# Optimization experiments

Measured on AMD Instinct MI355X. Metric: run time of the kernel, lower is better.

The kernel has to match this reference:

```python
import jax, jax.numpy as jnp
import numpy as np

NEG_INF = -9e15  # matches torch's -9000000000000000.0 mask fill
LEAKY_SLOPE = 0.01  # F.leaky_relu default


def setup_inputs() -> dict:
    key = jax.random.key(0)
    ks = jax.random.split(key, 6)
    B, N, F_in, F_out = 4, 4096, 256, 128
    h = jax.random.normal(ks[0], (B, N, F_in), dtype=jnp.float32)
    adj = jax.random.randint(ks[1], (B, N, N), 0, 2, dtype=jnp.int32)
    W_w = jax.random.normal(ks[2], (F_out, F_in), dtype=jnp.float32) * (1.0 / np.sqrt(F_in))
    W_b = jax.random.normal(ks[3], (F_out,), dtype=jnp.float32) * 0.01
    a_w = jax.random.normal(ks[4], (2 * F_out,), dtype=jnp.float32) * (1.0 / np.sqrt(2 * F_out))
    a_b = jax.random.normal(ks[5], (), dtype=jnp.float32) * 0.01
    return {"h": h, "adj": adj, "W_w": W_w, "W_b": W_b, "a_w": a_w, "a_b": a_b}


def reference(h, adj, W_w, W_b, a_w, a_b):
    # Wh: [B, N, F_out]
    Wh = jnp.einsum('bnf,of->bno', h, W_w) + W_b
    F_out = Wh.shape[-1]
    # a([Wh_i, Wh_j]) decomposes as a_src.Wh_i + a_dst.Wh_j + a_b (linearity),
    # avoiding the O(N^2 * 2F) repeat+cat intermediate while computing identical math.
    a_src, a_dst = a_w[:F_out], a_w[F_out:]
    src = jnp.einsum('bno,o->bn', Wh, a_src)  # [B, N]
    dst = jnp.einsum('bno,o->bn', Wh, a_dst)  # [B, N]
    e = src[:, :, None] + dst[:, None, :] + a_b  # [B, N, N]
    e = jnp.where(e >= 0, e, LEAKY_SLOPE * e)  # leaky_relu
    masked = jnp.where(adj > 0, e, NEG_INF)
    attention = jax.nn.softmax(masked, axis=-1)  # row softmax over neighbors j
    h_prime = jnp.einsum('bij,bjo->bio', attention, Wh)
    return h_prime
```

## Files before the change

kernel.cpp:

```cpp
#include <hip/hip_runtime.h>
#include <hip/hip_bf16.h>

typedef __attribute__((ext_vector_type(4))) float f32x4;
typedef __attribute__((ext_vector_type(8))) short s16x8;
typedef unsigned long long u64;

#define NB_ 4
#define N_ 4096
#define FI_ 256
#define FO_ 128
#define NROWS 16384
#define SPLIT 4
#define PHC 128
#define NST ((N_ / SPLIT) / PHC)

__device__ __forceinline__ unsigned pkbf(float a, float b) {
    __hip_bfloat162 t = __float22bfloat162_rn(make_float2(a, b));
    unsigned r; __builtin_memcpy(&r, &t, 4); return r;
}

typedef __attribute__((address_space(1))) const void CGV;
typedef __attribute__((address_space(3))) void LDSV;
__device__ __forceinline__ void gload16(const void* g, void* l) {
    __builtin_amdgcn_global_load_lds((CGV*)g, (LDSV*)l, 16, 0, 0);
}

__global__ __launch_bounds__(256) void k0_packw(
    const float* __restrict__ Ww, __hip_bfloat16* __restrict__ whi,
    __hip_bfloat16* __restrict__ wlo)
{
    int idx = blockIdx.x * 256 + threadIdx.x;
    float v = Ww[idx];
    __hip_bfloat16 hi = __float2bfloat16(v);
    whi[idx] = hi;
    wlo[idx] = __float2bfloat16(v - __bfloat162float(hi));
}

__global__ __launch_bounds__(256) void k1_wh(
    const float* __restrict__ h, const __hip_bfloat16* __restrict__ whi,
    const __hip_bfloat16* __restrict__ wlo, const float* __restrict__ Wb,
    const float* __restrict__ aw, const float* __restrict__ ab,
    short* __restrict__ WhTf, float* __restrict__ srcv,
    float* __restrict__ dstbv, unsigned* __restrict__ auxp)
{
    __shared__ float lds[16][132];
    const int tid = threadIdx.x;
    const int w = tid >> 6, l = tid & 63;
    const int lr = l & 15, g = l >> 4;
    const int r0 = blockIdx.x * 16;
    const float* hp = h + (size_t)(r0 + lr) * FI_ + g * 8;

    f32x4 acc[2] = {(f32x4)0.f, (f32x4)0.f};

    #pragma unroll
    for (int kt = 0; kt < 8; ++kt) {
        f32x4 x0 = *(const f32x4*)(hp + kt * 32);
        f32x4 x1 = *(const f32x4*)(hp + kt * 32 + 4);
        float xx[8];
        #pragma unroll
        for (int t = 0; t < 4; ++t) { xx[t] = x0[t]; xx[t + 4] = x1[t]; }
        union { s16x8 v; unsigned u[4]; } ahi, alo;
        #pragma unroll
        for (int t = 0; t < 4; ++t) {
            float a0 = xx[2 * t], a1 = xx[2 * t + 1];
            unsigned uh = pkbf(a0, a1);
            ahi.u[t] = uh;
            float h0f = __uint_as_float(uh << 16);
            float h1f = __uint_as_float(uh & 0xffff0000u);
            alo.u[t] = pkbf(a0 - h0f, a1 - h1f);
        }
        #pragma unroll
        for (int c = 0; c < 2; ++c) {
            const int o = w * 32 + c * 16 + lr;
            s16x8 bh = *(const s16x8*)(whi + (size_t)o * FI_ + kt * 32 + g * 8);
            s16x8 bl = *(const s16x8*)(wlo + (size_t)o * FI_ + kt * 32 + g * 8);
            acc[c] = __builtin_amdgcn_mfma_f32_16x16x32_bf16(ahi.v, bh, acc[c], 0, 0, 0);
            acc[c] = __builtin_amdgcn_mfma_f32_16x16x32_bf16(alo.v, bh, acc[c], 0, 0, 0);
            acc[c] = __builtin_amdgcn_mfma_f32_16x16x32_bf16(ahi.v, bl, acc[c], 0, 0, 0);
        }
    }

    #pragma unroll
    for (int c = 0; c < 2; ++c) {
        int col = w * 32 + c * 16 + lr;
        float wb = Wb[col];
        #pragma unroll
        for (int kk = 0; kk < 4; ++kk)
            lds[g * 4 + kk][col] = acc[c][kk] + wb;
    }
    __syncthreads();

    {
        const int o = tid >> 1, joct = tid & 1;
        const int jblk = (r0 & 4095) >> 5;
        const int bb = r0 >> 12;
        const int lb = ((r0 >> 3) & 3) + joct;
        union { s16x8 v; unsigned u[4]; } af;
        #pragma unroll
        for (int q = 0; q < 4; ++q)
            af.u[q] = pkbf(lds[joct * 8 + 2 * q][o], lds[joct * 8 + 2 * q + 1][o]);
        short* dst = WhTf + (((size_t)bb * 128 + jblk) * 8 + (o >> 4)) * 512
                          + ((o & 15) + 16 * lb) * 8;
        *(s16x8*)dst = af.v;
    }

    {
        const int row = tid >> 4, seg = tid & 15;
        float sp = 0.f, dp = 0.f;
        #pragma unroll
        for (int i = 0; i < 8; ++i) {
            float v = lds[row][seg * 8 + i];
            sp += v * aw[seg * 8 + i];
            dp += v * aw[FO_ + seg * 8 + i];
        }
        #pragma unroll
        for (int off = 8; off >= 1; off >>= 1) {
            sp += __shfl_xor(sp, off);
            dp += __shfl_xor(dp, off);
        }
        if (seg == 0) {
            int r = r0 + row;
            srcv[r] = sp;
            float db = dp + ab[0];
            dstbv[r] = db;
            auxp[r] = pkbf(__expf(db), __expf(0.01f * db));
        }
    }
}

__global__ __launch_bounds__(256) void k2b_max(
    const float* __restrict__ dstbv, float* __restrict__ maxv)
{
    const int b = blockIdx.x;
    const int t = threadIdx.x, w = t >> 6, l = t & 63;
    float m = -3.4e38f;
    for (int i = t; i < N_; i += 256) m = fmaxf(m, dstbv[b * N_ + i]);
    #pragma unroll
    for (int off = 32; off >= 1; off >>= 1) m = fmaxf(m, __shfl_xor(m, off));
    __shared__ float red[4];
    if (l == 0) red[w] = m;
    __syncthreads();
    if (t == 0) maxv[b] = fmaxf(fmaxf(red[0], red[1]), fmaxf(red[2], red[3]));
}

__global__ __launch_bounds__(256, 4) void k3_gat(
    const int* __restrict__ adj, const short* __restrict__ WhTf,
    const float* __restrict__ srcv, const unsigned* __restrict__ auxp,
    const float* __restrict__ maxv, float* __restrict__ pacc,
    float* __restrict__ prow)
{
    __shared__ int adjb[2][32][128];
    __shared__ float rsum[32];

    const int t = threadIdx.x;
    const int w = t >> 6, l = t & 63;
    const int lr = l & 15, g = l >> 4;
    const int rh = w & 1, oh = w >> 1;
    const int b = blockIdx.x >> 7;
    const int rblk = (blockIdx.x & 127) * 32;
    const int bN = b * N_;
    const int j0 = blockIdx.y * (N_ / SPLIT);

    float C1, C2;
    {
        int r = rblk + rh * 16 + lr;
        float s = srcv[bN + r];
        float eub = s + maxv[b];
        float m = fmaxf(eub, 0.01f * eub);
        C1 = __expf(s - m);
        C2 = __expf(0.01f * s - m);
    }

    const unsigned* axp = auxp + (size_t)bN + j0 + g * 8;
    const short* whsrc = WhTf + ((size_t)b * 128 + (j0 >> 5)) * 4096;

    f32x4 acc[4];
    #pragma unroll
    for (int ot = 0; ot < 4; ++ot) acc[ot] = (f32x4)0.f;
    float rs = 0.f;

    auto stage_adj = [&](int bi, int s) {
        const int jb = j0 + s * PHC;
        #pragma unroll
        for (int i = 0; i < 4; ++i) {
            int slot = i * 64 + (t & 63) + (t >> 6) * 256;
            int r = (i * 256 + t) >> 5;
            int c = (i * 256 + t) & 31;
            const int* src = adj + (size_t)(bN + rblk + r) * N_ + jb
                                 + ((c ^ (r & 7)) << 2);
            (void)slot;
            gload16(src, &adjb[bi][0][0] + (size_t)(i * 256 + w * 64) * 4);
        }
    };

    stage_adj(0, 0);
    __syncthreads();
    int cur = 0;

    for (int s = 0; s < NST; ++s) {
        if (s + 1 < NST) stage_adj(cur ^ 1, s + 1);

        #pragma unroll
        for (int js = 0; js < 4; ++js) {
            const int jc = s * PHC + js * 32;
            uint4 x0 = *(const uint4*)(axp + jc);
            uint4 x1 = *(const uint4*)(axp + jc + 4);
            const short* bp = whsrc + (size_t)(s * 4 + js) * 4096;
            s16x8 Bf[4];
            #pragma unroll
            for (int ot = 0; ot < 4; ++ot)
                Bf[ot] = *(const s16x8*)(bp + (oh * 4 + ot) * 512 + l * 8);

            const int R = rh * 16 + lr;
            const int c0 = js * 8 + 2 * g;
            const int4 a0 = *(const int4*)&adjb[cur][R][(c0 ^ (R & 7)) << 2];
            const int4 a1 = *(const int4*)&adjb[cur][R][((c0 + 1) ^ (R & 7)) << 2];

            const unsigned ax[8] = {x0.x, x0.y, x0.z, x0.w, x1.x, x1.y, x1.z, x1.w};
            const int av[8] = {a0.x, a0.y, a0.z, a0.w, a1.x, a1.y, a1.z, a1.w};
            float p[8];
            #pragma unroll
            for (int e = 0; e < 8; ++e) {
                float e1f = __uint_as_float(ax[e] << 16);
                float e2f = __uint_as_float(ax[e] & 0xffff0000u);
                float v = fmaxf(e1f * C1, e2f * C2);
                p[e] = (av[e] > 0) ? v : 0.f;
                rs += p[e];
            }
            union { s16x8 v; unsigned u[4]; } af;
            af.u[0] = pkbf(p[0], p[1]); af.u[1] = pkbf(p[2], p[3]);
            af.u[2] = pkbf(p[4], p[5]); af.u[3] = pkbf(p[6], p[7]);

            #pragma unroll
            for (int ot = 0; ot < 4; ++ot)
                acc[ot] = __builtin_amdgcn_mfma_f32_16x16x32_bf16(
                    af.v, Bf[ot], acc[ot], 0, 0, 0);
        }

        __syncthreads();
        cur ^= 1;
    }

    rs += __shfl_xor(rs, 16);
    rs += __shfl_xor(rs, 32);
    if (oh == 0 && l < 16) rsum[rh * 16 + l] = rs;
    __syncthreads();

    const size_t sb = (size_t)blockIdx.y * ((size_t)NROWS * FO_);
    #pragma unroll
    for (int kk = 0; kk < 4; ++kk) {
        int rloc = rh * 16 + g * 4 + kk;
        int grow = bN + rblk + rloc;
        float* pp = pacc + sb + (size_t)grow * FO_ + oh * 64 + lr;
        #pragma unroll
        for (int ot = 0; ot < 4; ++ot)
            pp[ot * 16] = acc[ot][kk];
        if (oh == 0 && lr == 0)
            prow[blockIdx.y * NROWS + grow] = rsum[rloc];
    }
}

__global__ __launch_bounds__(256) void k4_comb(
    const float* __restrict__ pacc, const float* __restrict__ prow,
    float* __restrict__ out)
{
    const int idx = blockIdx.x * 256 + threadIdx.x;
    const int grow = idx >> 7;
    float s = 0.f, rs = 0.f;
    #pragma unroll
    for (int si = 0; si < SPLIT; ++si) {
        s  += pacc[(size_t)si * ((size_t)NROWS * FO_) + idx];
        rs += prow[si * NROWS + grow];
    }
    out[idx] = s / rs;
}

extern "C" void kernel_launch(void* const* d_in, const int* in_sizes, int n_in,
                              void* d_out, int out_size, void* d_ws, size_t ws_size,
                              hipStream_t stream)
{
    const float* h  = (const float*)d_in[0];
    const int* adj  = (const int*)d_in[1];
    const float* Ww = (const float*)d_in[2];
    const float* Wb = (const float*)d_in[3];
    const float* aw = (const float*)d_in[4];
    const float* ab = (const float*)d_in[5];
    float* out = (float*)d_out;

    char* wsb = (char*)d_ws;
    float* pacc          = (float*)wsb;
    short* WhTf          = (short*)(wsb + 33554432u);
    char* aux            = wsb + 37748736u;
    float* srcv          = (float*)(aux);
    float* dstbv         = (float*)(aux + (64u << 10));
    unsigned* auxp       = (unsigned*)(aux + (128u << 10));
    __hip_bfloat16* whi  = (__hip_bfloat16*)(aux + (192u << 10));
    __hip_bfloat16* wlo  = (__hip_bfloat16*)(aux + (256u << 10));
    float* maxv          = (float*)(aux + (320u << 10));
    float* prow          = (float*)(aux + (384u << 10));

    k0_packw<<<128, 256, 0, stream>>>(Ww, whi, wlo);
    k1_wh<<<1024, 256, 0, stream>>>(h, whi, wlo, Wb, aw, ab, WhTf, srcv, dstbv, auxp);
    k2b_max<<<4, 256, 0, stream>>>(dstbv, maxv);
    dim3 g3(NB_ * 128, SPLIT);
    k3_gat<<<g3, 256, 0, stream>>>(adj, WhTf, srcv, auxp, maxv, pacc, prow);
    k4_comb<<<8192, 256, 0, stream>>>(pacc, prow, out);
}
```

Before: 142.9 us.

## Fuse dst max into Wh kernel via atomics and stage Wh/aux through LDS pipeline

Drops the separate max-reduction kernel: k1 now folds each block's dst max into a per-batch atomicMax on an order-preserving unsigned encoding, with a memset before launch. k3 moves to 32-column steps and stages adj (triple buffered), Wh tiles and aux values into LDS using async global-to-LDS loads, ordered with explicit vmcnt waits and barriers. This replaces direct global reads of B operands inside the loop. It also removes the LDS row-sum exchange by writing row sums directly. The aim is to hide global latency and save a launch, at the cost of one barrier per smaller step and hand-counted waitcnt correctness.

```diff
diff --git a/kernel.cpp b/kernel.cpp
--- a/kernel.cpp
+++ b/kernel.cpp
@@ -11,8 +11,7 @@
 #define FO_ 128
 #define NROWS 16384
 #define SPLIT 4
-#define PHC 128
-#define NST ((N_ / SPLIT) / PHC)
+#define NSTEPS ((N_ / SPLIT) / 32)
 
 __device__ __forceinline__ unsigned pkbf(float a, float b) {
     __hip_bfloat162 t = __float22bfloat162_rn(make_float2(a, b));
@@ -23,6 +22,15 @@
 typedef __attribute__((address_space(3))) void LDSV;
 __device__ __forceinline__ void gload16(const void* g, void* l) {
     __builtin_amdgcn_global_load_lds((CGV*)g, (LDSV*)l, 16, 0, 0);
+}
+
+__device__ __forceinline__ unsigned encf(float x) {
+    unsigned u = __float_as_uint(x);
+    return (u & 0x80000000u) ? ~u : (u | 0x80000000u);
+}
+__device__ __forceinline__ float decf(unsigned v) {
+    unsigned u = (v & 0x80000000u) ? (v ^ 0x80000000u) : ~v;
+    return __uint_as_float(u);
 }
 
 __global__ __launch_bounds__(256) void k0_packw(
@@ -41,9 +49,10 @@
     const __hip_bfloat16* __restrict__ wlo, const float* __restrict__ Wb,
     const float* __restrict__ aw, const float* __restrict__ ab,
     short* __restrict__ WhTf, float* __restrict__ srcv,
-    float* __restrict__ dstbv, unsigned* __restrict__ auxp)
+    unsigned* __restrict__ auxp, unsigned* __restrict__ maxenc)
 {
     __shared__ float lds[16][132];
+    __shared__ float dbsh[16];
     const int tid = threadIdx.x;
     const int w = tid >> 6, l = tid & 63;
     const int lr = l & 15, g = l >> 4;
@@ -122,35 +131,28 @@
             int r = r0 + row;
             srcv[r] = sp;
             float db = dp + ab[0];
-            dstbv[r] = db;
+            dbsh[row] = db;
             auxp[r] = pkbf(__expf(db), __expf(0.01f * db));
         }
-    }
-}
-
-__global__ __launch_bounds__(256) void k2b_max(
-    const float* __restrict__ dstbv, float* __restrict__ maxv)
-{
-    const int b = blockIdx.x;
-    const int t = threadIdx.x, w = t >> 6, l = t & 63;
-    float m = -3.4e38f;
-    for (int i = t; i < N_; i += 256) m = fmaxf(m, dstbv[b * N_ + i]);
-    #pragma unroll
-    for (int off = 32; off >= 1; off >>= 1) m = fmaxf(m, __shfl_xor(m, off));
-    __shared__ float red[4];
-    if (l == 0) red[w] = m;
-    __syncthreads();
-    if (t == 0) maxv[b] = fmaxf(fmaxf(red[0], red[1]), fmaxf(red[2], red[3]));
+        __syncthreads();
+        if (tid == 0) {
+            float m = dbsh[0];
+            #pragma unroll
+            for (int i = 1; i < 16; ++i) m = fmaxf(m, dbsh[i]);
+            atomicMax(&maxenc[r0 >> 12], encf(m));
+        }
+    }
 }
 
 __global__ __launch_bounds__(256, 4) void k3_gat(
     const int* __restrict__ adj, const short* __restrict__ WhTf,
     const float* __restrict__ srcv, const unsigned* __restrict__ auxp,
-    const float* __restrict__ maxv, float* __restrict__ pacc,
+    const unsigned* __restrict__ maxenc, float* __restrict__ pacc,
     float* __restrict__ prow)
 {
-    __shared__ int adjb[2][32][128];
-    __shared__ float rsum[32];
+    __shared__ int adjb[3][32][32];
+    __shared__ __hip_bfloat16 whb[2][4096];
+    __shared__ unsigned auxb[2][32];
 
     const int t = threadIdx.x;
     const int w = t >> 6, l = t & 63;
@@ -165,13 +167,13 @@
     {
         int r = rblk + rh * 16 + lr;
         float s = srcv[bN + r];
-        float eub = s + maxv[b];
+        float eub = s + decf(maxenc[b]);
         float m = fmaxf(eub, 0.01f * eub);
         C1 = __expf(s - m);
         C2 = __expf(0.01f * s - m);
     }
 
-    const unsigned* axp = auxp + (size_t)bN + j0 + g * 8;
+    const unsigned* axsrc = auxp + (size_t)bN + j0;
     const short* whsrc = WhTf + ((size_t)b * 128 + (j0 >> 5)) * 4096;
 
     f32x4 acc[4];
@@ -180,71 +182,82 @@
     float rs = 0.f;
 
     auto stage_adj = [&](int bi, int s) {
-        const int jb = j0 + s * PHC;
-        #pragma unroll
-        for (int i = 0; i < 4; ++i) {
-            int slot = i * 64 + (t & 63) + (t >> 6) * 256;
-            int r = (i * 256 + t) >> 5;
-            int c = (i * 256 + t) & 31;
-            const int* src = adj + (size_t)(bN + rblk + r) * N_ + jb
-                                 + ((c ^ (r & 7)) << 2);
-            (void)slot;
-            gload16(src, &adjb[bi][0][0] + (size_t)(i * 256 + w * 64) * 4);
-        }
+        const int jb = j0 + s * 32;
+        const int r = t >> 3, c = t & 7;
+        gload16(adj + (size_t)(bN + rblk + r) * N_ + jb + ((c ^ (r & 7)) << 2),
+                &adjb[bi][0][0] + w * 256);
     };
+    auto stage_wh = [&](int bi, int s) {
+        const short* src = whsrc + (size_t)s * 4096;
+        #pragma unroll
+        for (int i = 0; i < 2; ++i)
+            gload16(src + (size_t)(i * 256 + t) * 8,
+                    &whb[bi][0] + (size_t)(i * 256 + w * 64) * 8);
+    };
+    auto stage_aux = [&](int bi, int s) {
+        if (l < 2)
+            gload16(axsrc + s * 32 + (w * 2 + l) * 4, &auxb[bi][w * 8]);
+    };
 
     stage_adj(0, 0);
-    __syncthreads();
-    int cur = 0;
-
-    for (int s = 0; s < NST; ++s) {
-        if (s + 1 < NST) stage_adj(cur ^ 1, s + 1);
-
-        #pragma unroll
-        for (int js = 0; js < 4; ++js) {
-            const int jc = s * PHC + js * 32;
-            uint4 x0 = *(const uint4*)(axp + jc);
-            uint4 x1 = *(const uint4*)(axp + jc + 4);
-            const short* bp = whsrc + (size_t)(s * 4 + js) * 4096;
-            s16x8 Bf[4];
-            #pragma unroll
-            for (int ot = 0; ot < 4; ++ot)
-                Bf[ot] = *(const s16x8*)(bp + (oh * 4 + ot) * 512 + l * 8);
-
-            const int R = rh * 16 + lr;
-            const int c0 = js * 8 + 2 * g;
-            const int4 a0 = *(const int4*)&adjb[cur][R][(c0 ^ (R & 7)) << 2];
-            const int4 a1 = *(const int4*)&adjb[cur][R][((c0 + 1) ^ (R & 7)) << 2];
-
-            const unsigned ax[8] = {x0.x, x0.y, x0.z, x0.w, x1.x, x1.y, x1.z, x1.w};
-            const int av[8] = {a0.x, a0.y, a0.z, a0.w, a1.x, a1.y, a1.z, a1.w};
-            float p[8];
-            #pragma unroll
-            for (int e = 0; e < 8; ++e) {
-                float e1f = __uint_as_float(ax[e] << 16);
-                float e2f = __uint_as_float(ax[e] & 0xffff0000u);
-                float v = fmaxf(e1f * C1, e2f * C2);
-                p[e] = (av[e] > 0) ? v : 0.f;
-                rs += p[e];
-            }
-            union { s16x8 v; unsigned u[4]; } af;
-            af.u[0] = pkbf(p[0], p[1]); af.u[1] = pkbf(p[2], p[3]);
-            af.u[2] = pkbf(p[4], p[5]); af.u[3] = pkbf(p[6], p[7]);
-
-            #pragma unroll
-            for (int ot = 0; ot < 4; ++ot)
-                acc[ot] = __builtin_amdgcn_mfma_f32_16x16x32_bf16(
-                    af.v, Bf[ot], acc[ot], 0, 0, 0);
-        }
-
-        __syncthreads();
-        cur ^= 1;
+    __builtin_amdgcn_sched_barrier(0);
+    stage_aux(0, 0);
+    stage_wh(0, 0);
+    __builtin_amdgcn_sched_barrier(0);
+    stage_adj(1, 1);
+    __builtin_amdgcn_sched_barrier(0);
+
+    for (int s = 0; s < NSTEPS; ++s) {
+        __builtin_amdgcn_sched_barrier(0);
+        if (s + 1 < NSTEPS) asm volatile("s_waitcnt vmcnt(1)" ::: "memory");
+        else                asm volatile("s_waitcnt vmcnt(0)" ::: "memory");
+        __builtin_amdgcn_sched_barrier(0);
+        __builtin_amdgcn_s_barrier();
+        __builtin_amdgcn_sched_barrier(0);
+
+        const int cur = s & 1, curA = s % 3;
+        if (s + 1 < NSTEPS) {
+            stage_aux(cur ^ 1, s + 1);
+            stage_wh(cur ^ 1, s + 1);
+        }
+        if (s + 2 < NSTEPS) stage_adj((s + 2) % 3, s + 2);
+        __builtin_amdgcn_sched_barrier(0);
+
+        uint4 x0 = *(const uint4*)&auxb[cur][g * 8];
+        uint4 x1 = *(const uint4*)&auxb[cur][g * 8 + 4];
+        const int R = rh * 16 + lr;
+        const int4 a0 = *(const int4*)&adjb[curA][R][((2 * g) ^ (R & 7)) << 2];
+        const int4 a1 = *(const int4*)&adjb[curA][R][(((2 * g) + 1) ^ (R & 7)) << 2];
+        s16x8 Bf[4];
+        #pragma unroll
+        for (int ot = 0; ot < 4; ++ot)
+            Bf[ot] = *(const s16x8*)&whb[cur][(size_t)((oh * 4 + ot) * 64 + l) * 8];
+
+        const unsigned ax[8] = {x0.x, x0.y, x0.z, x0.w, x1.x, x1.y, x1.z, x1.w};
+        const int av[8] = {a0.x, a0.y, a0.z, a0.w, a1.x, a1.y, a1.z, a1.w};
+        float p[8];
+        #pragma unroll
+        for (int e = 0; e < 8; ++e) {
+            float e1f = __uint_as_float(ax[e] << 16);
+            float e2f = __uint_as_float(ax[e] & 0xffff0000u);
+            float v = fmaxf(e1f * C1, e2f * C2);
+            p[e] = (av[e] > 0) ? v : 0.f;
+            rs += p[e];
+        }
+        union { s16x8 v; unsigned u[4]; } af;
+        af.u[0] = pkbf(p[0], p[1]); af.u[1] = pkbf(p[2], p[3]);
+        af.u[2] = pkbf(p[4], p[5]); af.u[3] = pkbf(p[6], p[7]);
+
+        #pragma unroll
+        for (int ot = 0; ot < 4; ++ot)
+            acc[ot] = __builtin_amdgcn_mfma_f32_16x16x32_bf16(
+                af.v, Bf[ot], acc[ot], 0, 0, 0);
     }
 
     rs += __shfl_xor(rs, 16);
     rs += __shfl_xor(rs, 32);
-    if (oh == 0 && l < 16) rsum[rh * 16 + l] = rs;
-    __syncthreads();
+    if (oh == 0 && g == 0)
+        prow[blockIdx.y * NROWS + bN + rblk + rh * 16 + lr] = rs;
 
     const size_t sb = (size_t)blockIdx.y * ((size_t)NROWS * FO_);
     #pragma unroll
@@ -255,8 +268,6 @@
         #pragma unroll
         for (int ot = 0; ot < 4; ++ot)
             pp[ot * 16] = acc[ot][kk];
-        if (oh == 0 && lr == 0)
-            prow[blockIdx.y * NROWS + grow] = rsum[rloc];
     }
 }
 
@@ -292,17 +303,16 @@
     short* WhTf          = (short*)(wsb + 33554432u);
     char* aux            = wsb + 37748736u;
     float* srcv          = (float*)(aux);
-    float* dstbv         = (float*)(aux + (64u << 10));
-    unsigned* auxp       = (unsigned*)(aux + (128u << 10));
-    __hip_bfloat16* whi  = (__hip_bfloat16*)(aux + (192u << 10));
-    __hip_bfloat16* wlo  = (__hip_bfloat16*)(aux + (256u << 10));
-    float* maxv          = (float*)(aux + (320u << 10));
-    float* prow          = (float*)(aux + (384u << 10));
-
+    unsigned* auxp       = (unsigned*)(aux + (64u << 10));
+    __hip_bfloat16* whi  = (__hip_bfloat16*)(aux + (128u << 10));
+    __hip_bfloat16* wlo  = (__hip_bfloat16*)(aux + (192u << 10));
+    unsigned* maxenc     = (unsigned*)(aux + (256u << 10));
+    float* prow          = (float*)(aux + (320u << 10));
+
+    hipMemsetAsync(maxenc, 0, NB_ * sizeof(unsigned), stream);
     k0_packw<<<128, 256, 0, stream>>>(Ww, whi, wlo);
-    k1_wh<<<1024, 256, 0, stream>>>(h, whi, wlo, Wb, aw, ab, WhTf, srcv, dstbv, auxp);
-    k2b_max<<<4, 256, 0, stream>>>(dstbv, maxv);
+    k1_wh<<<1024, 256, 0, stream>>>(h, whi, wlo, Wb, aw, ab, WhTf, srcv, auxp, maxenc);
     dim3 g3(NB_ * 128, SPLIT);
-    k3_gat<<<g3, 256, 0, stream>>>(adj, WhTf, srcv, auxp, maxv, pacc, prow);
+    k3_gat<<<g3, 256, 0, stream>>>(adj, WhTf, srcv, auxp, maxenc, pacc, prow);
     k4_comb<<<8192, 256, 0, stream>>>(pacc, prow, out);
 }
```

Result: slower. 146.7 us (+2.6%).
